# Performance work log

Hardware: AMD Instinct MI355X
Metric: run time of the kernel (lower is better)

Reference implementation:

```python
import jax, jax.numpy as jnp
import numpy as np

EPS = 1e-6

def _normalize(x, axis):
    # torch F.normalize with eps: x / max(||x||_2, eps)
    n = jnp.linalg.norm(x, axis=axis, keepdims=True)
    return x / jnp.maximum(n, EPS)

def setup_inputs() -> dict:
    key = jax.random.key(0)
    ks = jax.random.split(key, 6)
    B, C, H, W = 16, 512, 32, 32
    N, D = 16384, 32
    return {
        "encodings": jax.random.normal(ks[0], (B, C, H, W), dtype=jnp.float32),
        "emb_weight": jax.random.normal(ks[1], (N, D), dtype=jnp.float32),
        "proj_w": jax.random.normal(ks[2], (D, C), dtype=jnp.float32) * 0.05,
        "proj_b": jax.random.normal(ks[3], (D,), dtype=jnp.float32) * 0.05,
        "exp_w": jax.random.normal(ks[4], (C, D), dtype=jnp.float32) * 0.05,
        "exp_b": jax.random.normal(ks[5], (C,), dtype=jnp.float32) * 0.05,
    }

def reference(encodings, emb_weight, proj_w, proj_b, exp_w, exp_b):
    N = emb_weight.shape[0]
    # projection: 1x1 conv == channel matmul; z: [B, D, H, W]
    z = jnp.einsum('bchw,dc->bdhw', encodings, proj_w) + proj_b[None, :, None, None]
    z = _normalize(z, axis=1)
    e = _normalize(emb_weight, axis=1)  # [N, D]
    # cosine similarities [B, N, H, W] -> nearest code per position
    sims = jnp.einsum('bdhw,nd->bnhw', z, e)
    idx = jnp.argmax(sims, axis=1)  # [B, H, W] int
    latents = jnp.transpose(e[idx], (0, 3, 1, 2))  # [B, D, H, W]
    loss_quantization = jnp.mean(jnp.square(z - latents))
    # straight-through estimator
    latents = z + jax.lax.stop_gradient(latents - z)
    out = jnp.einsum('bdhw,cd->bchw', latents, exp_w) + exp_b[None, :, None, None]
    # usage histogram -> perplexity
    flat = idx.ravel()
    usages = jnp.zeros((N,), dtype=jnp.float32).at[flat].add(1.0) / flat.shape[0]
    perplexity = jnp.exp(jnp.sum(-usages * jnp.log(usages + 1e-6)))
    return out, loss_quantization, perplexity
```

## Files before the change

### kernel.cpp

```cpp
#include <hip/hip_runtime.h>
#include <cstdint>

#define BATCH   16
#define CCH     512
#define DD      32
#define NCODES  16384
#define HWSZ    1024
#define P_TOTAL 16384
#define NCHUNK  16
#define CHUNK   (NCODES / NCHUNK)

typedef _Float16 half8 __attribute__((ext_vector_type(8)));
typedef float    f32x4 __attribute__((ext_vector_type(4)));

union H8 { _Float16 h[8]; uint4 u; };
union L8 { uint4 u; half8 h; };


__global__ __launch_bounds__(256) void prep_kernel(
    const float* __restrict__ enc, const float* __restrict__ pw,
    const float* __restrict__ pb, const float* __restrict__ emb,
    float* __restrict__ z, float* __restrict__ invz, char* __restrict__ zf16,
    float* __restrict__ en, char* __restrict__ ef16,
    int* __restrict__ hist, float* __restrict__ scalarAcc)
{
    const int t = threadIdx.x;

    if (blockIdx.x >= 320) {
        const int i = (blockIdx.x - 320) * 256 + t;
        hist[i] = 0;
        if (blockIdx.x == 320 && t < 2) scalarAcc[t] = 0.f;
        return;
    }

    if (blockIdx.x >= 256) {
        const int r = (blockIdx.x - 256) * 256 + t;
        const float4* src = reinterpret_cast<const float4*>(emb + (size_t)r * DD);
        float4 v[8];
        float ssq = 0.f;
#pragma unroll
        for (int q = 0; q < 8; q++) {
            v[q] = src[q];
            ssq += v[q].x * v[q].x + v[q].y * v[q].y + v[q].z * v[q].z + v[q].w * v[q].w;
        }
        const float inv = 1.f / fmaxf(sqrtf(ssq), 1e-6f);
        float4* dst = reinterpret_cast<float4*>(en + (size_t)r * DD);
        char* row = ef16 + (size_t)r * 128;
#pragma unroll
        for (int q = 0; q < 8; q += 2) {
            H8 hi, lo;
#pragma unroll
            for (int u = 0; u < 2; u++) {
                float4 o;
                o.x = v[q + u].x * inv; o.y = v[q + u].y * inv;
                o.z = v[q + u].z * inv; o.w = v[q + u].w * inv;
                dst[q + u] = o;
                const float s[4] = {o.x * 4096.f, o.y * 4096.f, o.z * 4096.f, o.w * 4096.f};
#pragma unroll
                for (int j = 0; j < 4; j++) {
                    const _Float16 h = (_Float16)s[j];
                    hi.h[u * 4 + j] = h;
                    lo.h[u * 4 + j] = (_Float16)(s[j] - (float)h);
                }
            }
            *(uint4*)(row + q * 8)      = hi.u;
            *(uint4*)(row + 64 + q * 8) = lo.u;
        }
        return;
    }

    const int hw_l = t & 63;
    const int dg   = __builtin_amdgcn_readfirstlane(t >> 6);
    const int p0   = blockIdx.x * 64;
    const int b    = p0 >> 10;
    const int hw   = (p0 & 1023) + hw_l;
    const float* encb = enc + (size_t)b * (CCH * HWSZ) + hw;

    float acc[8];
#pragma unroll
    for (int j = 0; j < 8; j++) acc[j] = 0.f;

    for (int c0 = 0; c0 < CCH; c0 += 16) {
        float ev[16];
#pragma unroll
        for (int u = 0; u < 16; u++)
            ev[u] = encb[(size_t)(c0 + u) * HWSZ];
#pragma unroll
        for (int u = 0; u < 16; u++)
#pragma unroll
            for (int j = 0; j < 8; j++)
                acc[j] = fmaf(ev[u], pw[(dg * 8 + j) * CCH + c0 + u], acc[j]);
    }

    const int p = p0 + hw_l;
    float ssq = 0.f;
    H8 hi, lo;
#pragma unroll
    for (int j = 0; j < 8; j++) {
        const float v = acc[j] + pb[dg * 8 + j];
        z[(size_t)p * DD + dg * 8 + j] = v;
        ssq = fmaf(v, v, ssq);
        const float vs = v * 4096.f;
        const _Float16 h = (_Float16)vs;
        hi.h[j] = h;
        lo.h[j] = (_Float16)(vs - (float)h);
    }
    char* row = zf16 + (size_t)p * 128;
    *(uint4*)(row + dg * 16)      = hi.u;
    *(uint4*)(row + 64 + dg * 16) = lo.u;

    __shared__ float red[4][64];
    red[dg][hw_l] = ssq;
    __syncthreads();
    if (t < 64) {
        const float tot = red[0][t] + red[1][t] + red[2][t] + red[3][t];
        invz[p0 + t] = 1.f / fmaxf(sqrtf(tot), 1e-6f);
    }
}

__global__ __launch_bounds__(256) void argmax_kernel(
    const char* __restrict__ zf16, const char* __restrict__ ef16,
    float* __restrict__ pval, int* __restrict__ pidx)
{
    const int w    = threadIdx.x >> 6;
    const int lane = threadIdx.x & 63;
    const int col  = lane & 15;
    const int quad = lane >> 4;
    const int pg    = blockIdx.x & 63;
    const int chunk = blockIdx.x >> 6;
    const int wp0   = pg * 256 + w * 64;

    half8 bh[4], bl[4];
#pragma unroll
    for (int tt = 0; tt < 4; tt++) {
        const char* r = zf16 + (size_t)(wp0 + tt * 16 + col) * 128 + quad * 16;
        L8 a; a.u = *(const uint4*)(r);       bh[tt] = a.h;
        L8 b; b.u = *(const uint4*)(r + 64);  bl[tt] = b.h;
    }

    const int n0 = chunk * CHUNK;
    const char* abase = ef16 + (size_t)(n0 + col) * 128 + quad * 16;

    float best[4] = {-3e38f, -3e38f, -3e38f, -3e38f};
    int   bidx[4] = {0, 0, 0, 0};
    int   code = n0 + quad * 4;

    uint4 pa_h = *(const uint4*)(abase);
    uint4 pa_l = *(const uint4*)(abase + 64);
    const f32x4 zero4 = {0.f, 0.f, 0.f, 0.f};

    for (int tile = 0; tile < CHUNK / 16; tile++) {
        L8 ahu, alu;
        ahu.u = pa_h;
        alu.u = pa_l;
        const char* nxt = abase + (size_t)(tile + 1) * 2048;
        pa_h = *(const uint4*)(nxt);
        pa_l = *(const uint4*)(nxt + 64);

        const half8 ah = ahu.h, al = alu.h;

        f32x4 acc[4];
#pragma unroll
        for (int tt = 0; tt < 4; tt++)
            acc[tt] = __builtin_amdgcn_mfma_f32_16x16x32_f16(ah, bh[tt], zero4, 0, 0, 0);
#pragma unroll
        for (int tt = 0; tt < 4; tt++)
            acc[tt] = __builtin_amdgcn_mfma_f32_16x16x32_f16(ah, bl[tt], acc[tt], 0, 0, 0);
#pragma unroll
        for (int tt = 0; tt < 4; tt++)
            acc[tt] = __builtin_amdgcn_mfma_f32_16x16x32_f16(al, bh[tt], acc[tt], 0, 0, 0);
#pragma unroll
        for (int tt = 0; tt < 4; tt++)
            acc[tt] = __builtin_amdgcn_mfma_f32_16x16x32_f16(al, bl[tt], acc[tt], 0, 0, 0);

#pragma unroll
        for (int tt = 0; tt < 4; tt++)
#pragma unroll
            for (int r = 0; r < 4; r++) {
                const float v = acc[tt][r];
                if (v > best[tt]) { best[tt] = v; bidx[tt] = code + r; }
            }
        code += 16;
    }

#pragma unroll
    for (int off = 16; off < 64; off <<= 1) {
#pragma unroll
        for (int tt = 0; tt < 4; tt++) {
            const float ov = __shfl_xor(best[tt], off);
            const int   oi = __shfl_xor(bidx[tt], off);
            if (ov > best[tt] || (ov == best[tt] && oi < bidx[tt])) {
                best[tt] = ov; bidx[tt] = oi;
            }
        }
    }
    if (quad == 0) {
#pragma unroll
        for (int tt = 0; tt < 4; tt++) {
            pval[(size_t)chunk * P_TOTAL + wp0 + tt * 16 + col] = best[tt];
            pidx[(size_t)chunk * P_TOTAL + wp0 + tt * 16 + col] = bidx[tt];
        }
    }
}

__global__ __launch_bounds__(64) void combine_kernel(
    const float* __restrict__ pval, const int* __restrict__ pidx,
    const float* __restrict__ z, const float* __restrict__ invz,
    const float* __restrict__ en,
    int* __restrict__ idx, int* __restrict__ hist, float* __restrict__ scalarAcc)
{
    const int p = blockIdx.x * 64 + threadIdx.x;
    float best = -3e38f;
    int   bi   = 0;
#pragma unroll
    for (int k = 0; k < NCHUNK; k++) {
        const float v = pval[k * P_TOTAL + p];
        const int   i = pidx[k * P_TOTAL + p];
        if (v > best) { best = v; bi = i; }
    }
    idx[p] = bi;
    atomicAdd(&hist[bi], 1);

    const float iv = invz[p];
    const float4* zsrc = reinterpret_cast<const float4*>(z + (size_t)p * DD);
    const float4* esrc = reinterpret_cast<const float4*>(en + (size_t)bi * DD);
    float ls = 0.f;
#pragma unroll
    for (int q = 0; q < 8; q++) {
        const float4 zv = zsrc[q];
        const float4 ev = esrc[q];
        const float dx = zv.x * iv - ev.x;
        const float dy = zv.y * iv - ev.y;
        const float dz = zv.z * iv - ev.z;
        const float dw = zv.w * iv - ev.w;
        ls += dx * dx + dy * dy + dz * dz + dw * dw;
    }
    __shared__ float red[64];
    red[threadIdx.x] = ls;
    __syncthreads();
    for (int s = 32; s > 0; s >>= 1) {
        if (threadIdx.x < s) red[threadIdx.x] += red[threadIdx.x + s];
        __syncthreads();
    }
    if (threadIdx.x == 0) atomicAdd(&scalarAcc[0], red[0]);
}

__global__ __launch_bounds__(256) void expand_kernel(
    const int* __restrict__ idx, const float* __restrict__ en,
    const float* __restrict__ ew, const float* __restrict__ eb,
    float* __restrict__ out)
{
    const int t     = threadIdx.x;
    const int chalf = blockIdx.x & 1;
    const int pg    = blockIdx.x >> 1;
    const int p0    = pg * 64;
    const int b     = p0 >> 10;
    const int hw0   = p0 & 1023;

    __shared__ float lat[64 * 33];
    for (int i = t; i < 64 * DD; i += 256) {
        const int pl = i >> 5, d = i & 31;
        lat[pl * 33 + d] = en[(size_t)idx[p0 + pl] * DD + d];
    }
    __syncthreads();

    const int hw_l = t & 63;
    const int cg   = __builtin_amdgcn_readfirstlane(t >> 6);
    float lr[32];
#pragma unroll
    for (int d = 0; d < DD; d++) lr[d] = lat[hw_l * 33 + d];

    float* outb = out + (size_t)b * (CCH * HWSZ) + hw0 + hw_l;
    const int c0 = chalf * 256 + cg * 64;
#pragma unroll 4
    for (int k = 0; k < 64; k++) {
        const int c = c0 + k;
        const float* ewc = ew + (size_t)c * DD;
        float s0 = 0.f, s1 = 0.f, s2 = 0.f, s3 = 0.f;
#pragma unroll
        for (int d = 0; d < DD; d += 4) {
            s0 = fmaf(lr[d + 0], ewc[d + 0], s0);
            s1 = fmaf(lr[d + 1], ewc[d + 1], s1);
            s2 = fmaf(lr[d + 2], ewc[d + 2], s2);
            s3 = fmaf(lr[d + 3], ewc[d + 3], s3);
        }
        outb[(size_t)c * HWSZ] = (s0 + s1) + (s2 + s3) + eb[c];
    }
}

__global__ __launch_bounds__(256) void entropy_kernel(
    const int* __restrict__ hist, float* __restrict__ scalarAcc)
{
    const int i = blockIdx.x * 256 + threadIdx.x;
    const float u = (float)hist[i] * (1.f / (float)P_TOTAL);
    float h = -u * logf(u + 1e-6f);
    __shared__ float red[256];
    red[threadIdx.x] = h;
    __syncthreads();
    for (int s = 128; s > 0; s >>= 1) {
        if (threadIdx.x < s) red[threadIdx.x] += red[threadIdx.x + s];
        __syncthreads();
    }
    if (threadIdx.x == 0) atomicAdd(&scalarAcc[1], red[0]);
}

__global__ __launch_bounds__(64) void scalar_kernel(
    const float* __restrict__ scalarAcc, float* __restrict__ out_scalars)
{
    if (threadIdx.x == 0) {
        out_scalars[0] = scalarAcc[0] * (1.f / (float)(P_TOTAL * DD));
        out_scalars[1] = expf(scalarAcc[1]);
    }
}

extern "C" void kernel_launch(void* const* d_in, const int* in_sizes, int n_in,
                              void* d_out, int out_size, void* d_ws, size_t ws_size,
                              hipStream_t stream)
{
    const float* enc = (const float*)d_in[0];
    const float* emb = (const float*)d_in[1];
    const float* pw  = (const float*)d_in[2];
    const float* pb  = (const float*)d_in[3];
    const float* ew  = (const float*)d_in[4];
    const float* eb  = (const float*)d_in[5];
    float* out = (float*)d_out;

    char* ws = (char*)d_ws;
    float* z         = (float*)(ws + 0);
    float* invz      = (float*)(ws + 2097152);
    float* en        = (float*)(ws + 2162688);
    char*  zf16      = ws + 4259840;
    char*  ef16      = ws + 6356992;
    float* pval      = (float*)(ws + 8454144);
    int*   pidx      = (int*)  (ws + 9502720);
    int*   idx       = (int*)  (ws + 10551296);
    int*   hist      = (int*)  (ws + 10616832);
    float* scalarAcc = (float*)(ws + 10682368);

    prep_kernel   <<<384, 256, 0, stream>>>(enc, pw, pb, emb, z, invz, zf16,
                                            en, ef16, hist, scalarAcc);
    argmax_kernel <<<64 * NCHUNK, 256, 0, stream>>>(zf16, ef16, pval, pidx);
    combine_kernel<<<P_TOTAL / 64, 64, 0, stream>>>(pval, pidx, z, invz, en,
                                                    idx, hist, scalarAcc);
    entropy_kernel<<<NCODES / 256, 256, 0, stream>>>(hist, scalarAcc);
    expand_kernel <<<512, 256, 0, stream>>>(idx, en, ew, eb, out);
    scalar_kernel <<<1, 64, 0, stream>>>(scalarAcc, out + 8388608);
}
```

Measured before the change: 252.5 us.

## Fuse combine with expand, split codebook finer, deepen prefetch, drop scalar kernel

Several changes land at once. Argmax now splits the codebook into 32 chunks with a reordered block-to-chunk mapping, a two-deep prefetch of codebook tiles, and a launch-bounds occupancy hint. Combine and expand are fused into one 512-thread kernel that reduces the partial maxima in shared memory and fills the latent tile directly, so the idx buffer and its reload go away. The final scalar kernel is folded into the entropy kernel using a last-block atomic counter, and prep software-pipelines its encoding loads. Together these aim to cut launch count and global round trips and to keep more waves in flight, at the cost of extra partial-result traffic and a fused kernel with fewer blocks for the output stage.

```diff
diff --git a/kernel.cpp b/kernel.cpp
--- a/kernel.cpp
+++ b/kernel.cpp
@@ -7,7 +7,7 @@
 #define NCODES  16384
 #define HWSZ    1024
 #define P_TOTAL 16384
-#define NCHUNK  16
+#define NCHUNK  32
 #define CHUNK   (NCODES / NCHUNK)
 
 typedef _Float16 half8 __attribute__((ext_vector_type(8)));
@@ -29,7 +29,7 @@
     if (blockIdx.x >= 320) {
         const int i = (blockIdx.x - 320) * 256 + t;
         hist[i] = 0;
-        if (blockIdx.x == 320 && t < 2) scalarAcc[t] = 0.f;
+        if (blockIdx.x == 320 && t < 4) scalarAcc[t] = 0.f;
         return;
     }
 
@@ -80,17 +80,28 @@
 #pragma unroll
     for (int j = 0; j < 8; j++) acc[j] = 0.f;
 
-    for (int c0 = 0; c0 < CCH; c0 += 16) {
-        float ev[16];
+    float ev[16];
+#pragma unroll
+    for (int u = 0; u < 16; u++) ev[u] = encb[(size_t)u * HWSZ];
+
+    for (int c0 = 0; c0 < CCH - 16; c0 += 16) {
+        float nv[16];
 #pragma unroll
         for (int u = 0; u < 16; u++)
-            ev[u] = encb[(size_t)(c0 + u) * HWSZ];
+            nv[u] = encb[(size_t)(c0 + 16 + u) * HWSZ];
 #pragma unroll
         for (int u = 0; u < 16; u++)
 #pragma unroll
             for (int j = 0; j < 8; j++)
                 acc[j] = fmaf(ev[u], pw[(dg * 8 + j) * CCH + c0 + u], acc[j]);
-    }
+#pragma unroll
+        for (int u = 0; u < 16; u++) ev[u] = nv[u];
+    }
+#pragma unroll
+    for (int u = 0; u < 16; u++)
+#pragma unroll
+        for (int j = 0; j < 8; j++)
+            acc[j] = fmaf(ev[u], pw[(dg * 8 + j) * CCH + (CCH - 16) + u], acc[j]);
 
     const int p = p0 + hw_l;
     float ssq = 0.f;
@@ -118,7 +129,7 @@
     }
 }
 
-__global__ __launch_bounds__(256) void argmax_kernel(
+__global__ __launch_bounds__(256, 4) void argmax_kernel(
     const char* __restrict__ zf16, const char* __restrict__ ef16,
     float* __restrict__ pval, int* __restrict__ pidx)
 {
@@ -126,8 +137,8 @@
     const int lane = threadIdx.x & 63;
     const int col  = lane & 15;
     const int quad = lane >> 4;
-    const int pg    = blockIdx.x & 63;
-    const int chunk = blockIdx.x >> 6;
+    const int chunk = (blockIdx.x & 7) * 4 + (blockIdx.x >> 9);
+    const int pg    = (blockIdx.x >> 3) & 63;
     const int wp0   = pg * 256 + w * 64;
 
     half8 bh[4], bl[4];
@@ -145,17 +156,20 @@
     int   bidx[4] = {0, 0, 0, 0};
     int   code = n0 + quad * 4;
 
-    uint4 pa_h = *(const uint4*)(abase);
-    uint4 pa_l = *(const uint4*)(abase + 64);
+    uint4 p0h = *(const uint4*)(abase);
+    uint4 p0l = *(const uint4*)(abase + 64);
+    uint4 p1h = *(const uint4*)(abase + 2048);
+    uint4 p1l = *(const uint4*)(abase + 2048 + 64);
     const f32x4 zero4 = {0.f, 0.f, 0.f, 0.f};
 
     for (int tile = 0; tile < CHUNK / 16; tile++) {
         L8 ahu, alu;
-        ahu.u = pa_h;
-        alu.u = pa_l;
-        const char* nxt = abase + (size_t)(tile + 1) * 2048;
-        pa_h = *(const uint4*)(nxt);
-        pa_l = *(const uint4*)(nxt + 64);
+        ahu.u = p0h;
+        alu.u = p0l;
+        p0h = p1h; p0l = p1l;
+        const char* nxt = abase + (size_t)(tile + 2) * 2048;
+        p1h = *(const uint4*)(nxt);
+        p1l = *(const uint4*)(nxt + 64);
 
         const half8 ah = ahu.h, al = alu.h;
 
@@ -203,64 +217,71 @@
     }
 }
 
-__global__ __launch_bounds__(64) void combine_kernel(
+__global__ __launch_bounds__(512) void combex_kernel(
     const float* __restrict__ pval, const int* __restrict__ pidx,
     const float* __restrict__ z, const float* __restrict__ invz,
-    const float* __restrict__ en,
-    int* __restrict__ idx, int* __restrict__ hist, float* __restrict__ scalarAcc)
-{
-    const int p = blockIdx.x * 64 + threadIdx.x;
-    float best = -3e38f;
-    int   bi   = 0;
-#pragma unroll
-    for (int k = 0; k < NCHUNK; k++) {
-        const float v = pval[k * P_TOTAL + p];
-        const int   i = pidx[k * P_TOTAL + p];
-        if (v > best) { best = v; bi = i; }
-    }
-    idx[p] = bi;
-    atomicAdd(&hist[bi], 1);
-
-    const float iv = invz[p];
-    const float4* zsrc = reinterpret_cast<const float4*>(z + (size_t)p * DD);
-    const float4* esrc = reinterpret_cast<const float4*>(en + (size_t)bi * DD);
-    float ls = 0.f;
-#pragma unroll
-    for (int q = 0; q < 8; q++) {
-        const float4 zv = zsrc[q];
-        const float4 ev = esrc[q];
-        const float dx = zv.x * iv - ev.x;
-        const float dy = zv.y * iv - ev.y;
-        const float dz = zv.z * iv - ev.z;
-        const float dw = zv.w * iv - ev.w;
-        ls += dx * dx + dy * dy + dz * dz + dw * dw;
-    }
-    __shared__ float red[64];
-    red[threadIdx.x] = ls;
+    const float* __restrict__ en, const float* __restrict__ ew,
+    const float* __restrict__ eb,
+    int* __restrict__ hist, float* __restrict__ scalarAcc,
+    float* __restrict__ out)
+{
+    const int t  = threadIdx.x;
+    const int p0 = blockIdx.x * 64;
+
+    __shared__ float lat[64 * 33];
+    __shared__ float bvs[8][64];
+    __shared__ int   bis[8][64];
+
+    {
+        const int pl = t & 63;
+        const int kg = t >> 6;
+        const int p  = p0 + pl;
+        float best = -3e38f;
+        int   bi   = 0;
+#pragma unroll
+        for (int k = 0; k < 4; k++) {
+            const float v = pval[(size_t)(kg * 4 + k) * P_TOTAL + p];
+            const int   i = pidx[(size_t)(kg * 4 + k) * P_TOTAL + p];
+            if (v > best) { best = v; bi = i; }
+        }
+        bvs[kg][pl] = best;
+        bis[kg][pl] = bi;
+    }
     __syncthreads();
-    for (int s = 32; s > 0; s >>= 1) {
-        if (threadIdx.x < s) red[threadIdx.x] += red[threadIdx.x + s];
-        __syncthreads();
-    }
-    if (threadIdx.x == 0) atomicAdd(&scalarAcc[0], red[0]);
-}
-
-__global__ __launch_bounds__(256) void expand_kernel(
-    const int* __restrict__ idx, const float* __restrict__ en,
-    const float* __restrict__ ew, const float* __restrict__ eb,
-    float* __restrict__ out)
-{
-    const int t     = threadIdx.x;
-    const int chalf = blockIdx.x & 1;
-    const int pg    = blockIdx.x >> 1;
-    const int p0    = pg * 64;
-    const int b     = p0 >> 10;
-    const int hw0   = p0 & 1023;
-
-    __shared__ float lat[64 * 33];
-    for (int i = t; i < 64 * DD; i += 256) {
-        const int pl = i >> 5, d = i & 31;
-        lat[pl * 33 + d] = en[(size_t)idx[p0 + pl] * DD + d];
+
+    if (t < 64) {
+        float best = bvs[0][t];
+        int   bi   = bis[0][t];
+#pragma unroll
+        for (int kg = 1; kg < 8; kg++) {
+            const float v = bvs[kg][t];
+            const int   i = bis[kg][t];
+            if (v > best || (v == best && i < bi)) { best = v; bi = i; }
+        }
+        const int p = p0 + t;
+        atomicAdd(&hist[bi], 1);
+
+        const float iv = invz[p];
+        const float4* zsrc = reinterpret_cast<const float4*>(z + (size_t)p * DD);
+        const float4* esrc = reinterpret_cast<const float4*>(en + (size_t)bi * DD);
+        float ls = 0.f;
+#pragma unroll
+        for (int q = 0; q < 8; q++) {
+            const float4 zv = zsrc[q];
+            const float4 ev = esrc[q];
+            lat[t * 33 + q * 4 + 0] = ev.x;
+            lat[t * 33 + q * 4 + 1] = ev.y;
+            lat[t * 33 + q * 4 + 2] = ev.z;
+            lat[t * 33 + q * 4 + 3] = ev.w;
+            const float dx = zv.x * iv - ev.x;
+            const float dy = zv.y * iv - ev.y;
+            const float dz = zv.z * iv - ev.z;
+            const float dw = zv.w * iv - ev.w;
+            ls += dx * dx + dy * dy + dz * dz + dw * dw;
+        }
+#pragma unroll
+        for (int off = 32; off > 0; off >>= 1) ls += __shfl_down(ls, off);
+        if (t == 0) atomicAdd(&scalarAcc[0], ls);
     }
     __syncthreads();
 
@@ -270,8 +291,10 @@
 #pragma unroll
     for (int d = 0; d < DD; d++) lr[d] = lat[hw_l * 33 + d];
 
+    const int b   = p0 >> 10;
+    const int hw0 = p0 & 1023;
     float* outb = out + (size_t)b * (CCH * HWSZ) + hw0 + hw_l;
-    const int c0 = chalf * 256 + cg * 64;
+    const int c0 = cg * 64;
 #pragma unroll 4
     for (int k = 0; k < 64; k++) {
         const int c = c0 + k;
@@ -289,7 +312,8 @@
 }
 
 __global__ __launch_bounds__(256) void entropy_kernel(
-    const int* __restrict__ hist, float* __restrict__ scalarAcc)
+    const int* __restrict__ hist, float* __restrict__ scalarAcc,
+    float* __restrict__ out_scalars)
 {
     const int i = blockIdx.x * 256 + threadIdx.x;
     const float u = (float)hist[i] * (1.f / (float)P_TOTAL);
@@ -301,15 +325,19 @@
         if (threadIdx.x < s) red[threadIdx.x] += red[threadIdx.x + s];
         __syncthreads();
     }
-    if (threadIdx.x == 0) atomicAdd(&scalarAcc[1], red[0]);
-}
-
-__global__ __launch_bounds__(64) void scalar_kernel(
-    const float* __restrict__ scalarAcc, float* __restrict__ out_scalars)
-{
     if (threadIdx.x == 0) {
-        out_scalars[0] = scalarAcc[0] * (1.f / (float)(P_TOTAL * DD));
-        out_scalars[1] = expf(scalarAcc[1]);
+        atomicAdd(&scalarAcc[1], red[0]);
+        __threadfence();
+        int* cnt = (int*)(scalarAcc + 2);
+        const int prev = atomicAdd(cnt, 1);
+        if (prev == 63) {
+            const float loss = __hip_atomic_load(&scalarAcc[0], __ATOMIC_RELAXED,
+                                                 __HIP_MEMORY_SCOPE_AGENT);
+            const float ent  = __hip_atomic_load(&scalarAcc[1], __ATOMIC_RELAXED,
+                                                 __HIP_MEMORY_SCOPE_AGENT);
+            out_scalars[0] = loss * (1.f / (float)(P_TOTAL * DD));
+            out_scalars[1] = expf(ent);
+        }
     }
 }
 
@@ -332,17 +360,15 @@
     char*  zf16      = ws + 4259840;
     char*  ef16      = ws + 6356992;
     float* pval      = (float*)(ws + 8454144);
-    int*   pidx      = (int*)  (ws + 9502720);
-    int*   idx       = (int*)  (ws + 10551296);
-    int*   hist      = (int*)  (ws + 10616832);
-    float* scalarAcc = (float*)(ws + 10682368);
+    int*   pidx      = (int*)  (ws + 10551296);
+    int*   hist      = (int*)  (ws + 12648448);
+    float* scalarAcc = (float*)(ws + 12713984);
 
     prep_kernel   <<<384, 256, 0, stream>>>(enc, pw, pb, emb, z, invz, zf16,
                                             en, ef16, hist, scalarAcc);
     argmax_kernel <<<64 * NCHUNK, 256, 0, stream>>>(zf16, ef16, pval, pidx);
-    combine_kernel<<<P_TOTAL / 64, 64, 0, stream>>>(pval, pidx, z, invz, en,
-                                                    idx, hist, scalarAcc);
-    entropy_kernel<<<NCODES / 256, 256, 0, stream>>>(hist, scalarAcc);
-    expand_kernel <<<512, 256, 0, stream>>>(idx, en, ew, eb, out);
-    scalar_kernel <<<1, 64, 0, stream>>>(scalarAcc, out + 8388608);
-}
+    combex_kernel <<<P_TOTAL / 64, 512, 0, stream>>>(pval, pidx, z, invz, en,
+                                                     ew, eb, hist, scalarAcc, out);
+    entropy_kernel<<<NCODES / 256, 256, 0, stream>>>(hist, scalarAcc,
+                                                     out + 8388608);
+}
```

New measurement: 252.2 us. No clear change (-0.1%).
